# Optimization experiments

Hardware: AMD Instinct MI355X
Metric: run time of the kernel (lower is better)

The kernel has to match this reference:

```python
import jax, jax.numpy as jnp
import numpy as np

VOCAB = 100000; D = 300; F_NUM = 768
M = 64; N = 16
SURF_L = 4; CTX_L = 50; DOC_L = 100; BODY_L = 200
HEADS = 5


def _conv_relu_avg(x, W, b):
    # x: [B, L, D] tokens-embedded; conv1d (valid) + relu + global avgpool -> [B, F]
    y = jax.lax.conv_general_dilated(x.transpose(0, 2, 1), W, (1,), 'VALID',
                                     dimension_numbers=('NCH', 'OIH', 'NCH'))
    return jax.nn.relu(y + b[None, :, None]).mean(axis=2)


def _mha(q, k, v, num_heads=HEADS):
    # split-head scaled dot-product attention (no learned projections), q:[Lq,D] k,v:[Lk,D]
    Lq, Dm = q.shape
    hd = Dm // num_heads
    qh = q.reshape(Lq, num_heads, hd).transpose(1, 0, 2)
    kh = k.reshape(k.shape[0], num_heads, hd).transpose(1, 0, 2)
    vh = v.reshape(v.shape[0], num_heads, hd).transpose(1, 0, 2)
    att = jax.nn.softmax(jnp.einsum('hqd,hkd->hqk', qh, kh) * (1.0 / np.sqrt(hd)), axis=-1)
    out = jnp.einsum('hqk,hkd->hqd', att, vh)
    return out.transpose(1, 0, 2).reshape(Lq, Dm)


def _cos(a, b, eps=1e-6):
    na = jnp.maximum(jnp.sqrt((a * a).sum(-1)), eps)
    nb = jnp.maximum(jnp.sqrt((b * b).sum(-1)), eps)
    return (a * b).sum(-1) / (na * nb)


def setup_inputs() -> dict:
    key = jax.random.key(0)
    ks = jax.random.split(key, 20)
    inp = {}
    inp['mention_entity'] = jnp.ones((M, N), dtype=jnp.int32)
    inp['m'] = M
    inp['n'] = N
    inp['mention_vec'] = jax.random.randint(ks[0], (M, SURF_L), 0, VOCAB)
    inp['context_vec'] = jax.random.randint(ks[1], (M, CTX_L), 0, VOCAB)
    inp['doc_vec'] = jax.random.randint(ks[2], (DOC_L,), 0, VOCAB)
    inp['title_vec'] = jax.random.normal(ks[3], (N, F_NUM), dtype=jnp.float32)
    inp['body_vec'] = jax.random.randint(ks[4], (N, BODY_L), 0, VOCAB)
    inp['sfeats'] = jnp.zeros((N, 1), dtype=jnp.float32)
    inp['m2c_prior'] = jax.random.uniform(ks[5], (N,), dtype=jnp.float32)
    inp['men2cands'] = jax.random.randint(ks[6], (M, N), 0, VOCAB)
    inp['contexts_ids'] = jax.random.randint(ks[7], (M, CTX_L), 0, VOCAB)
    inp['hand_features'] = jax.random.uniform(ks[8], (N, 1), dtype=jnp.float32)
    inp['bert_doc_vec'] = jax.random.normal(ks[9], (1, F_NUM), dtype=jnp.float32)
    # learned parameters
    inp['embed_table'] = jax.random.normal(ks[10], (VOCAB, D), dtype=jnp.float32) * 0.1
    inp['conv_ms_w'] = jax.random.normal(ks[11], (F_NUM, D, 2), dtype=jnp.float32) * 0.05
    inp['conv_ms_b'] = jnp.zeros((F_NUM,), dtype=jnp.float32)
    inp['conv_mc_w'] = jax.random.normal(ks[12], (F_NUM, D, 5), dtype=jnp.float32) * 0.05
    inp['conv_mc_b'] = jnp.zeros((F_NUM,), dtype=jnp.float32)
    inp['layer_local_w'] = jax.random.normal(ks[13], (7,), dtype=jnp.float32) * 0.3
    inp['layer_local_b'] = jnp.zeros((), dtype=jnp.float32)
    inp['att_w1'] = jax.random.normal(ks[14], (600, 300), dtype=jnp.float32) * 0.05
    inp['att_b1'] = jnp.zeros((300,), dtype=jnp.float32)
    inp['att_w2'] = jax.random.normal(ks[15], (300, 1), dtype=jnp.float32) * 0.05
    inp['att_b2'] = jnp.zeros((), dtype=jnp.float32)
    return inp


def reference(mention_entity, m, n, mention_vec, context_vec, doc_vec, title_vec,
              body_vec, sfeats, m2c_prior, men2cands, contexts_ids, hand_features,
              bert_doc_vec, embed_table, conv_ms_w, conv_ms_b, conv_mc_w, conv_mc_b,
              layer_local_w, layer_local_b, att_w1, att_b1, att_w2, att_b2):
    # per-mention conv features (vectorized over all mentions at once)
    ms = _conv_relu_avg(embed_table[mention_vec], conv_ms_w, conv_ms_b)   # [M,768]
    mc = _conv_relu_avg(embed_table[context_vec], conv_mc_w, conv_mc_b)   # [M,768]
    md = bert_doc_vec[0]                                                  # [768]
    doc_emb = embed_table[doc_vec]                                        # [100,300]
    body_emb = embed_table[body_vec]                                      # [N,200,300]

    # per-candidate cross attention doc<->body, max-pooled over query positions
    att_d_b = jax.vmap(lambda b: _mha(doc_emb, b, b).max(axis=0))(body_emb)          # [N,300]
    att_b_d = jax.vmap(lambda b: _mha(b, doc_emb, doc_emb).max(axis=0))(body_emb)    # [N,300]
    comb = jnp.concatenate([att_d_b, att_b_d], axis=-1)                              # [N,600]
    att_score = jax.nn.sigmoid(jax.nn.relu(comb @ att_w1 + att_b1) @ att_w2 + att_b2)[:, 0]  # [N]

    # LocalCtxAttRanker: candidate-vs-context attention score
    ctx_emb = embed_table[contexts_ids]                                   # [M,50,300]
    cand_emb = embed_table[men2cands]                                     # [M,N,300]
    tok = jnp.einsum('mnd,mtd->mnt', cand_emb, ctx_emb)                   # [M,N,50]
    p = jax.nn.softmax(tok.max(axis=1), axis=-1)                          # [M,50]
    ctxv = jnp.einsum('mt,mtd->md', p, ctx_emb)                           # [M,300]
    local_att = jnp.einsum('mnd,md->mn', cand_emb, ctxv)                  # [M,N]

    cos_st = _cos(ms[:, None, :], title_vec[None, :, :])                  # [M,N]
    cos_dt = _cos(md[None, :], title_vec)                                 # [N]
    cos_ct = _cos(mc[:, None, :], title_vec[None, :, :])                  # [M,N]

    Mm = ms.shape[0]
    bc = lambda v: jnp.broadcast_to(v[None, :], (Mm, v.shape[0]))
    # feature order matches torch.cat((hand_fea, prior, localAtt, attScore, C_score))
    feats = jnp.stack([bc(hand_features[:, 0]), bc(m2c_prior), local_att,
                       bc(att_score), cos_st, bc(cos_dt), cos_ct], axis=-1)  # [M,N,7]
    score = feats @ layer_local_w + layer_local_b                         # [M,N]

    # per-mention standardization (unbiased std, as torch.std), softmax and uniform renorm
    mu = score.mean(axis=1, keepdims=True)
    sd = score.std(axis=1, keepdims=True, ddof=1)
    z = (score - mu) / sd
    sm = jax.nn.softmax(z, axis=1)
    zmin = z.min(axis=1, keepdims=True)
    zmax = z.max(axis=1, keepdims=True)
    u = (z + 1.0 - zmin) / (zmax - zmin)
    u = u / u.sum(axis=1, keepdims=True)
    return (z, sm, u)
```

## Files before the change

### kernel.cpp

```cpp
#include <hip/hip_runtime.h>

#define MM 64
#define NN 16
#define DDIM 300
#define FNUM 768
#define SURF_LL 4
#define CTX_LL 50
#define DOC_LL 100
#define BODY_LL 200
#define NHEADS 5
#define HDIM 60

#define GM 2944
#define GK 1536
#define GN 768

typedef unsigned short u16;
typedef unsigned int u32;
typedef __attribute__((ext_vector_type(8))) short short8;
typedef __attribute__((ext_vector_type(4))) float f32x4;

#define OFF_MSG    0
#define OFF_CTX2G  76800
#define OFF_CANDG  1036800
#define OFF_MS     1344000
#define OFF_MC     1393152
#define OFF_PV0    1442304
#define OFF_PV1    1461504
#define OFF_ASC    1495104
#define OFF_LATT   1495120
#define OFF_ABF    1496144
#define OFF_WTMC   (OFF_ABF + GM*GK/2)
#define OFF_WTMS   (OFF_WTMC + GN*GK/2)

__device__ __forceinline__ u16 f2bf(float x) {
  union { float f; u32 u; } v; v.f = x;
  u32 r = v.u + 0x7FFFu + ((v.u >> 16) & 1u);
  return (u16)(r >> 16);
}

__device__ __forceinline__ float rdlane(float x, int l) {
  return __uint_as_float(__builtin_amdgcn_readlane(__float_as_uint(x), l));
}

__global__ __launch_bounds__(256) void mega_prep_kernel(
    const float* __restrict__ embed,
    const int* __restrict__ mention_vec,
    const int* __restrict__ context_vec,
    const int* __restrict__ contexts_ids,
    const int* __restrict__ men2cands,
    const float* __restrict__ Wmc,
    const float* __restrict__ Wms,
    float* __restrict__ dst, float* __restrict__ mc,
    float* __restrict__ att_logit,
    u32* __restrict__ Abf, u32* __restrict__ WTmc, float* __restrict__ WTms) {
  int bid = blockIdx.x;
  if (bid < 5250) {
    int e = bid * 256 + threadIdx.x;
    int row = e / DDIM;
    int col = e - row * DDIM;
    int tok;
    if (row < 256)       tok = mention_vec[row];
    else if (row < 3456) tok = contexts_ids[row - 256];
    else                 tok = men2cands[row - 3456];
    dst[e] = embed[(size_t)tok * DDIM + col];
  } else if (bid < 5442) {
    mc[(bid - 5250) * 256 + threadIdx.x] = 0.f;
  } else if (bid == 5442) {
    if (threadIdx.x < NN) att_logit[threadIdx.x] = 0.f;
  } else if (bid < 14275) {
    int idx = (bid - 5443) * 256 + threadIdx.x;
    int r = idx / (GK / 2);
    int kp = idx - r * (GK / 2);
    int k = kp * 2;
    int m = r / 46, t = r - m * 46;
    u32 out = 0;
#pragma unroll
    for (int j = 0; j < 2; j++) {
      int kj = k + j;
      u16 h = 0;
      if (kj < 1500) {
        int tap = kj / 300;
        int d = kj - tap * 300;
        int tok = context_vec[m * CTX_LL + t + tap];
        h = f2bf(embed[(size_t)tok * DDIM + d]);
      }
      out |= (u32)h << (16 * j);
    }
    Abf[idx] = out;
  } else if (bid < 16579) {
    int idx = (bid - 14275) * 256 + threadIdx.x;
    int n = idx / (GK / 2);
    int kp = idx - n * (GK / 2);
    int k = kp * 2;
    u32 out = 0;
#pragma unroll
    for (int j = 0; j < 2; j++) {
      int kj = k + j;
      u16 h = 0;
      if (kj < 1500) {
        int tap = kj / 300;
        int d = kj - tap * 300;
        h = f2bf(Wmc[(size_t)n * 1500 + d * 5 + tap]);
      }
      out |= (u32)h << (16 * j);
    }
    WTmc[idx] = out;
  } else {
    int idx = (bid - 16579) * 256 + threadIdx.x;
    int k = idx / FNUM;
    int f = idx - k * FNUM;
    WTms[idx] = Wms[(size_t)f * 600 + k];
  }
}

__global__ __launch_bounds__(256) void conv_gemm_kernel(
    const u16* __restrict__ A,
    const u16* __restrict__ B,
    const float* __restrict__ bias,
    float* __restrict__ mc) {
  int bn = blockIdx.x, bm = blockIdx.y;
  __shared__ u16 As[64][72];
  __shared__ u16 Bs[64][72];
  int tid = threadIdx.x;
  int w = tid >> 6, lane = tid & 63;
  int wr = w >> 1, wc = w & 1;
  int lg = lane >> 4, lm = lane & 15;
  f32x4 acc[2][2];
#pragma unroll
  for (int i = 0; i < 2; i++)
#pragma unroll
    for (int j = 0; j < 2; j++) acc[i][j] = (f32x4)0.f;
  int c0row = tid >> 3, ck = (tid & 7) * 8;
  const u16* Ag = A + (size_t)(bm * 64) * GK;
  const u16* Bg = B + (size_t)(bn * 64) * GK;
  for (int kt = 0; kt < GK / 64; kt++) {
    int k0 = kt * 64;
    uint4 av0 = *(const uint4*)(Ag + (size_t)c0row * GK + k0 + ck);
    uint4 av1 = *(const uint4*)(Ag + (size_t)(c0row + 32) * GK + k0 + ck);
    uint4 bv0 = *(const uint4*)(Bg + (size_t)c0row * GK + k0 + ck);
    uint4 bv1 = *(const uint4*)(Bg + (size_t)(c0row + 32) * GK + k0 + ck);
    __syncthreads();
    *(uint4*)&As[c0row][ck] = av0;
    *(uint4*)&As[c0row + 32][ck] = av1;
    *(uint4*)&Bs[c0row][ck] = bv0;
    *(uint4*)&Bs[c0row + 32][ck] = bv1;
    __syncthreads();
#pragma unroll
    for (int kk = 0; kk < 2; kk++) {
      short8 af0 = *(const short8*)&As[wr * 32 + lm][kk * 32 + lg * 8];
      short8 af1 = *(const short8*)&As[wr * 32 + 16 + lm][kk * 32 + lg * 8];
      short8 bf0 = *(const short8*)&Bs[wc * 32 + lm][kk * 32 + lg * 8];
      short8 bf1 = *(const short8*)&Bs[wc * 32 + 16 + lm][kk * 32 + lg * 8];
      acc[0][0] = __builtin_amdgcn_mfma_f32_16x16x32_bf16(af0, bf0, acc[0][0], 0, 0, 0);
      acc[0][1] = __builtin_amdgcn_mfma_f32_16x16x32_bf16(af0, bf1, acc[0][1], 0, 0, 0);
      acc[1][0] = __builtin_amdgcn_mfma_f32_16x16x32_bf16(af1, bf0, acc[1][0], 0, 0, 0);
      acc[1][1] = __builtin_amdgcn_mfma_f32_16x16x32_bf16(af1, bf1, acc[1][1], 0, 0, 0);
    }
  }
#pragma unroll
  for (int mf = 0; mf < 2; mf++)
#pragma unroll
    for (int nf = 0; nf < 2; nf++) {
      int col = bn * 64 + wc * 32 + nf * 16 + lm;
      float bb = bias[col];
      int base = bm * 64 + wr * 32 + mf * 16 + lg * 4;
      int mcur = base / 46;
      float s = 0.f;
#pragma unroll
      for (int r = 0; r < 4; r++) {
        float v = fmaxf(acc[mf][nf][r] + bb, 0.f) * (1.0f / 46.0f);
        int mm = (base + r) / 46;
        if (mm != mcur) { atomicAdd(&mc[mcur * FNUM + col], s); s = 0.f; mcur = mm; }
        s += v;
      }
      atomicAdd(&mc[mcur * FNUM + col], s);
    }
}

__device__ __forceinline__ void conv_ms_body(
    const float* __restrict__ msg, const float* __restrict__ WT,
    const float* __restrict__ B, float* __restrict__ ms, int b) {
  int m = b / 3, fi = b - m * 3;
  int f = fi * 256 + threadIdx.x;
  const float* x = msg + m * SURF_LL * DDIM;
  float a0 = 0.f, a1 = 0.f, a2 = 0.f;
  for (int d = 0; d < DDIM; d++) {
    float v0 = x[d], v1 = x[DDIM + d], v2 = x[2 * DDIM + d], v3 = x[3 * DDIM + d];
    float wA = WT[(size_t)(2 * d) * FNUM + f];
    float wB = WT[(size_t)(2 * d + 1) * FNUM + f];
    a0 += v0 * wA + v1 * wB;
    a1 += v1 * wA + v2 * wB;
    a2 += v2 * wA + v3 * wB;
  }
  float bb = B[f];
  float r = fmaxf(a0 + bb, 0.f) + fmaxf(a1 + bb, 0.f) + fmaxf(a2 + bb, 0.f);
  ms[m * FNUM + f] = r * (1.0f / 3.0f);
}

template <int DIR>
__device__ __forceinline__ void scores_pv_body(
    const float* __restrict__ embed, const int* __restrict__ doc_vec,
    const int* __restrict__ body_vec, float* __restrict__ pvp, int b,
    float* __restrict__ smem) {
  constexpr int Lq = DIR ? 200 : 100;
  constexpr int NT = DIR ? 1 : 2;
  constexpr int NQT = DIR ? 7 : 4;
  int qt = b / 80;
  int rem = b - qt * 80;
  int n = rem / 5, h = rem - n * 5;
  const int* qids = DIR ? body_vec + n * BODY_LL : doc_vec;
  const int* kids = DIR ? doc_vec : body_vec + n * BODY_LL;
  float* Ks = smem;
  float* Qs = smem + 6200;
  float* red = smem + 8248;
  for (int idx = threadIdx.x; idx < 32 * 15; idx += 256) {
    int r = idx / 15, c = idx - r * 15;
    int q = qt * 32 + r; if (q >= Lq) q = Lq - 1;
    float4 v = *(const float4*)(embed + (size_t)qids[q] * DDIM + h * HDIM + c * 4);
    float* dp = Qs + r * 64 + c * 4;
    dp[0] = v.x; dp[1] = v.y; dp[2] = v.z; dp[3] = v.w;
  }
  int w = threadIdx.x >> 6, lane = threadIdx.x & 63;
  int dl = (lane < HDIM) ? lane : (HDIM - 1);
  const float scale = 0.12909944487358056f;
  float mrun[8], srun[8], O[8];
#pragma unroll
  for (int i = 0; i < 8; i++) { mrun[i] = -1e30f; srun[i] = 0.f; O[i] = 0.f; }
  int kc0 = lane;
  int kc1 = (lane + 64 < 100) ? lane + 64 : 99;
  bool v1ok = (lane + 64 < 100);
  for (int kt = 0; kt < NT; kt++) {
    if (kt > 0) __syncthreads();
    for (int idx = threadIdx.x; idx < 100 * 15; idx += 256) {
      int r = idx / 15, c = idx - r * 15;
      float4 v = *(const float4*)(embed + (size_t)kids[kt * 100 + r] * DDIM + h * HDIM + c * 4);
      float* dp = Ks + r * 62 + c * 4;
      dp[0] = v.x; dp[1] = v.y; dp[2] = v.z; dp[3] = v.w;
    }
    __syncthreads();
    float acc[8][2];
#pragma unroll
    for (int i = 0; i < 8; i++) { acc[i][0] = 0.f; acc[i][1] = 0.f; }
    for (int d = 0; d < HDIM; d += 4) {
      float2 a0 = *(const float2*)&Ks[kc0 * 62 + d];
      float2 b0 = *(const float2*)&Ks[kc0 * 62 + d + 2];
      float2 a1 = *(const float2*)&Ks[kc1 * 62 + d];
      float2 b1 = *(const float2*)&Ks[kc1 * 62 + d + 2];
#pragma unroll
      for (int i = 0; i < 8; i++) {
        float4 qv = *(const float4*)&Qs[(w * 8 + i) * 64 + d];
        acc[i][0] += qv.x * a0.x + qv.y * a0.y + qv.z * b0.x + qv.w * b0.y;
        acc[i][1] += qv.x * a1.x + qv.y * a1.y + qv.z * b1.x + qv.w * b1.y;
      }
    }
#pragma unroll
    for (int i = 0; i < 8; i++) {
      float v0 = acc[i][0] * scale;
      float v1 = v1ok ? acc[i][1] * scale : -1e30f;
      float tm = fmaxf(v0, v1);
#pragma unroll
      for (int o = 32; o >= 1; o >>= 1) tm = fmaxf(tm, __shfl_xor(tm, o));
      float mn = fmaxf(mrun[i], tm);
      float fsc = __expf(mrun[i] - mn);
      float p0 = __expf(v0 - mn);
      float p1 = v1ok ? __expf(v1 - mn) : 0.f;
      float ts = p0 + p1;
#pragma unroll
      for (int o = 32; o >= 1; o >>= 1) ts += __shfl_xor(ts, o);
      srun[i] = srun[i] * fsc + ts;
      mrun[i] = mn;
      O[i] *= fsc;
      acc[i][0] = p0; acc[i][1] = p1;
    }
#pragma unroll 4
    for (int k = 0; k < 64; k++) {
      float vk = Ks[k * 62 + dl];
#pragma unroll
      for (int i = 0; i < 8; i++) O[i] += rdlane(acc[i][0], k) * vk;
    }
#pragma unroll 4
    for (int k = 64; k < 100; k++) {
      float vk = Ks[k * 62 + dl];
#pragma unroll
      for (int i = 0; i < 8; i++) O[i] += rdlane(acc[i][1], k - 64) * vk;
    }
  }
  float omax = -1e30f;
#pragma unroll
  for (int i = 0; i < 8; i++) {
    int q = qt * 32 + w * 8 + i;
    if (q < Lq) omax = fmaxf(omax, O[i] / srun[i]);
  }
  red[w * 64 + lane] = omax;
  __syncthreads();
  if (threadIdx.x < 64 && lane < HDIM) {
    float m4 = fmaxf(fmaxf(red[0 * 64 + lane], red[1 * 64 + lane]),
                     fmaxf(red[2 * 64 + lane], red[3 * 64 + lane]));
    pvp[((size_t)(n * NHEADS + h) * NQT + qt) * HDIM + lane] = m4;
  }
}

__device__ __forceinline__ void tokctxv_body(
    const float* __restrict__ candg, const float* __restrict__ ctx2g,
    float* __restrict__ local_att, int m, float* __restrict__ smem) {
  float* ctx   = smem;
  float* tokb  = smem + 4800;
  float* tkmx  = smem + 5072;
  float* pp    = smem + 5136;
  float* sctxv = smem + 5200;
  int tid = threadIdx.x;
  int nI = tid >> 4, tt = tid & 15;
  const float* cand = candg + (size_t)m * NN * DDIM;
  for (int tile = 0; tile < 4; tile++) {
    int cbase = tile * 16;
    __syncthreads();
    for (int i = tid; i < 16 * DDIM; i += 256) {
      int rr = i / DDIM, cc = i - rr * DDIM;
      int t = cbase + rr;
      ctx[rr * DDIM + cc] = (t < CTX_LL) ? ctx2g[(size_t)(m * CTX_LL + t) * DDIM + cc] : 0.f;
    }
    __syncthreads();
    const float4* ca = (const float4*)(cand + nI * DDIM);
    const float4* cb = (const float4*)(ctx + tt * DDIM);
    float dsum = 0.f;
#pragma unroll
    for (int c = 0; c < 75; c++) {
      float4 a = ca[c], b = cb[c];
      dsum += a.x * b.x + a.y * b.y + a.z * b.z + a.w * b.w;
    }
    tokb[nI * 17 + tt] = dsum;
    __syncthreads();
    if (tid < 16) {
      float mx = -1e30f;
      for (int nn = 0; nn < NN; nn++) mx = fmaxf(mx, tokb[nn * 17 + tid]);
      int t = cbase + tid;
      if (t < CTX_LL) tkmx[t] = mx;
    }
  }
  __syncthreads();
  if (tid < 64) {
    float v = (tid < CTX_LL) ? tkmx[tid] : -1e30f;
    float mx = v;
#pragma unroll
    for (int o = 32; o >= 1; o >>= 1) mx = fmaxf(mx, __shfl_xor(mx, o));
    float e = (tid < CTX_LL) ? expf(v - mx) : 0.f;
    float s = e;
#pragma unroll
    for (int o = 32; o >= 1; o >>= 1) s += __shfl_xor(s, o);
    pp[tid] = e / s;
  }
  __syncthreads();
  for (int d = tid; d < DDIM; d += 256) {
    float acc = 0.f;
    for (int t = 0; t < CTX_LL; t++)
      acc += pp[t] * ctx2g[(size_t)(m * CTX_LL + t) * DDIM + d];
    sctxv[d] = acc;
  }
  __syncthreads();
  int j = tid & 15;
  float dd = 0.f;
  for (int i = j; i < DDIM; i += 16) dd += cand[nI * DDIM + i] * sctxv[i];
#pragma unroll
  for (int o = 8; o >= 1; o >>= 1) dd += __shfl_xor(dd, o);
  if (j == 0) local_att[m * NN + nI] = dd;
}

__global__ __launch_bounds__(256, 4) void mega_mid_kernel(
    const float* __restrict__ embed,
    const int* __restrict__ doc_vec,
    const int* __restrict__ body_vec,
    const float* __restrict__ msg,
    const float* __restrict__ WTms,
    const float* __restrict__ Bms,
    const float* __restrict__ candg,
    const float* __restrict__ ctx2g,
    float* __restrict__ ms,
    float* __restrict__ pv0,
    float* __restrict__ pv1,
    float* __restrict__ local_att) {
  __shared__ float smem[8504];
  int bid = blockIdx.x;
  if (bid < 192) {
    conv_ms_body(msg, WTms, Bms, ms, bid);
  } else if (bid < 512) {
    scores_pv_body<0>(embed, doc_vec, body_vec, pv0, bid - 192, smem);
  } else if (bid < 1072) {
    scores_pv_body<1>(embed, doc_vec, body_vec, pv1, bid - 512, smem);
  } else {
    tokctxv_body(candg, ctx2g, local_att, bid - 1072, smem);
  }
}

__global__ __launch_bounds__(256) void mlp_kernel(
    const float* __restrict__ pv0, const float* __restrict__ pv1,
    const float* __restrict__ w1, const float* __restrict__ b1,
    const float* __restrict__ w2,
    float* __restrict__ att_logit) {
  int bid = blockIdx.x;
  int n = bid / 5, jc = bid - n * 5;
  int tid = threadIdx.x;
  __shared__ float comb[600];
  __shared__ float partial[4][64];
  for (int idx = tid; idx < 600; idx += 256) {
    int side = idx >= 300;
    int pos = idx - side * 300;
    int h = pos / 60, d = pos - h * 60;
    float mx = -1e30f;
    if (!side) {
#pragma unroll
      for (int pt = 0; pt < 4; pt++)
        mx = fmaxf(mx, pv0[(size_t)((n * NHEADS + h) * 4 + pt) * HDIM + d]);
    } else {
#pragma unroll
      for (int pt = 0; pt < 7; pt++)
        mx = fmaxf(mx, pv1[(size_t)((n * NHEADS + h) * 7 + pt) * HDIM + d]);
    }
    comb[idx] = mx;
  }
  __syncthreads();
  int w = tid >> 6, lane = tid & 63;
  int jl = (lane < 60) ? lane : 59;
  int jg = jc * 60 + jl;
  float acc = 0.f;
  for (int k = w; k < 600; k += 4)
    acc += comb[k] * w1[(size_t)k * 300 + jg];
  partial[w][lane] = acc;
  __syncthreads();
  if (tid < 64) {
    float hv = partial[0][lane] + partial[1][lane] +
               partial[2][lane] + partial[3][lane];
    float hj = fmaxf(hv + b1[jg], 0.f) * w2[jg];
    if (lane >= 60) hj = 0.f;
#pragma unroll
    for (int o = 32; o >= 1; o >>= 1) hj += __shfl_xor(hj, o);
    if (lane == 0) atomicAdd(&att_logit[n], hj);
  }
}

__global__ __launch_bounds__(256) void final_kernel(
    const float* __restrict__ ms,
    const float* __restrict__ mc,
    const float* __restrict__ title,
    const float* __restrict__ bert,
    const float* __restrict__ att_logit,
    const float* __restrict__ b2,
    const float* __restrict__ m2c_prior,
    const float* __restrict__ hand,
    const float* __restrict__ local_att,
    const float* __restrict__ w7,
    const float* __restrict__ b7,
    float* __restrict__ out) {
  int m = blockIdx.x, tid = threadIdx.x;
  __shared__ float sms[FNUM], smc[FNUM], smd[FNUM];
  __shared__ float snorm[3], sscore[16], wred[3][4];
  for (int i = tid; i < FNUM; i += 256) {
    sms[i] = ms[m * FNUM + i];
    smc[i] = mc[m * FNUM + i];
    smd[i] = bert[i];
  }
  __syncthreads();
  float p1 = 0.f, p2 = 0.f, p3 = 0.f;
  for (int i = tid; i < FNUM; i += 256) {
    float a = sms[i], b = smc[i], c = smd[i];
    p1 += a * a; p2 += b * b; p3 += c * c;
  }
#pragma unroll
  for (int o = 32; o >= 1; o >>= 1) {
    p1 += __shfl_xor(p1, o); p2 += __shfl_xor(p2, o); p3 += __shfl_xor(p3, o);
  }
  int wid = tid >> 6, lane = tid & 63;
  if (lane == 0) { wred[0][wid] = p1; wred[1][wid] = p2; wred[2][wid] = p3; }
  __syncthreads();
  if (tid == 0) {
    snorm[0] = fmaxf(sqrtf(wred[0][0] + wred[0][1] + wred[0][2] + wred[0][3]), 1e-6f);
    snorm[1] = fmaxf(sqrtf(wred[1][0] + wred[1][1] + wred[1][2] + wred[1][3]), 1e-6f);
    snorm[2] = fmaxf(sqrtf(wred[2][0] + wred[2][1] + wred[2][2] + wred[2][3]), 1e-6f);
  }
  __syncthreads();
  int nI = tid >> 4, j = tid & 15;
  float d1 = 0.f, d2 = 0.f, d3 = 0.f, d4 = 0.f;
  for (int i = j; i < FNUM; i += 16) {
    float t = title[nI * FNUM + i];
    d1 += sms[i] * t; d2 += smc[i] * t; d3 += smd[i] * t; d4 += t * t;
  }
#pragma unroll
  for (int o = 8; o >= 1; o >>= 1) {
    d1 += __shfl_xor(d1, o); d2 += __shfl_xor(d2, o);
    d3 += __shfl_xor(d3, o); d4 += __shfl_xor(d4, o);
  }
  if (j == 0) {
    float nt = fmaxf(sqrtf(d4), 1e-6f);
    float cos_st = d1 / (snorm[0] * nt);
    float cos_ct = d2 / (snorm[1] * nt);
    float cos_dt = d3 / (snorm[2] * nt);
    float asc = 1.0f / (1.0f + expf(-(att_logit[nI] + b2[0])));
    float score = hand[nI] * w7[0] + m2c_prior[nI] * w7[1] +
                  local_att[m * NN + nI] * w7[2] + asc * w7[3] +
                  cos_st * w7[4] + cos_dt * w7[5] + cos_ct * w7[6] + b7[0];
    sscore[nI] = score;
  }
  __syncthreads();
  if (tid < 16) {
    float x = sscore[tid];
    float s = x;
#pragma unroll
    for (int o = 8; o >= 1; o >>= 1) s += __shfl_xor(s, o);
    float mu = s * (1.0f / 16.0f);
    float dv = (x - mu) * (x - mu);
    float vs = dv;
#pragma unroll
    for (int o = 8; o >= 1; o >>= 1) vs += __shfl_xor(vs, o);
    float sd = sqrtf(vs * (1.0f / 15.0f));
    float z = (x - mu) / sd;
    float zm = z;
#pragma unroll
    for (int o = 8; o >= 1; o >>= 1) zm = fmaxf(zm, __shfl_xor(zm, o));
    float e = expf(z - zm);
    float es = e;
#pragma unroll
    for (int o = 8; o >= 1; o >>= 1) es += __shfl_xor(es, o);
    float sm = e / es;
    float zmin = z;
#pragma unroll
    for (int o = 8; o >= 1; o >>= 1) zmin = fminf(zmin, __shfl_xor(zmin, o));
    float u0 = (z + 1.0f - zmin) / (zm - zmin);
    float us = u0;
#pragma unroll
    for (int o = 8; o >= 1; o >>= 1) us += __shfl_xor(us, o);
    float u = u0 / us;
    out[m * NN + tid] = z;
    out[MM * NN + m * NN + tid] = sm;
    out[2 * MM * NN + m * NN + tid] = u;
  }
}

extern "C" void kernel_launch(void* const* d_in, const int* in_sizes, int n_in,
                              void* d_out, int out_size, void* d_ws, size_t ws_size,
                              hipStream_t stream) {
  const int*   mention_vec   = (const int*)d_in[3];
  const int*   context_vec   = (const int*)d_in[4];
  const int*   doc_vec       = (const int*)d_in[5];
  const float* title_vec     = (const float*)d_in[6];
  const int*   body_vec      = (const int*)d_in[7];
  const float* m2c_prior     = (const float*)d_in[9];
  const int*   men2cands     = (const int*)d_in[10];
  const int*   contexts_ids  = (const int*)d_in[11];
  const float* hand_features = (const float*)d_in[12];
  const float* bert_doc_vec  = (const float*)d_in[13];
  const float* embed_table   = (const float*)d_in[14];
  const float* conv_ms_w     = (const float*)d_in[15];
  const float* conv_ms_b     = (const float*)d_in[16];
  const float* conv_mc_w     = (const float*)d_in[17];
  const float* conv_mc_b     = (const float*)d_in[18];
  const float* layer_local_w = (const float*)d_in[19];
  const float* layer_local_b = (const float*)d_in[20];
  const float* att_w1        = (const float*)d_in[21];
  const float* att_b1        = (const float*)d_in[22];
  const float* att_w2        = (const float*)d_in[23];
  const float* att_b2        = (const float*)d_in[24];

  float* ws     = (float*)d_ws;
  float* msg    = ws + OFF_MSG;
  float* ctx2g  = ws + OFF_CTX2G;
  float* candg  = ws + OFF_CANDG;
  float* ms     = ws + OFF_MS;
  float* mc     = ws + OFF_MC;
  float* pv0    = ws + OFF_PV0;
  float* pv1    = ws + OFF_PV1;
  float* att_lg = ws + OFF_ASC;
  float* latt   = ws + OFF_LATT;
  u16*   Abf    = (u16*)(ws + OFF_ABF);
  u16*   WTmc   = (u16*)(ws + OFF_WTMC);
  float* WTms   = ws + OFF_WTMS;
  float* out    = (float*)d_out;

  mega_prep_kernel<<<dim3(18379), dim3(256), 0, stream>>>(
      embed_table, mention_vec, context_vec, contexts_ids, men2cands,
      conv_mc_w, conv_ms_w, ws, mc, att_lg, (u32*)Abf, (u32*)WTmc, WTms);
  conv_gemm_kernel<<<dim3(GN / 64, GM / 64), dim3(256), 0, stream>>>(
      Abf, WTmc, conv_mc_b, mc);
  mega_mid_kernel<<<dim3(1136), dim3(256), 0, stream>>>(
      embed_table, doc_vec, body_vec, msg, WTms, conv_ms_b, candg, ctx2g,
      ms, pv0, pv1, latt);
  mlp_kernel<<<dim3(80), dim3(256), 0, stream>>>(
      pv0, pv1, att_w1, att_b1, att_w2, att_lg);
  final_kernel<<<dim3(MM), dim3(256), 0, stream>>>(
      ms, mc, title_vec, bert_doc_vec, att_lg, att_b2, m2c_prior,
      hand_features, latt, layer_local_w, layer_local_b, out);
}
```

Baseline: 439.3 us.

## Replace online softmax and readlane PV with two-pass softmax and LDS-staged probabilities

The attention body now computes all QK scores before any softmax, holding every score tile in registers. It then does a single exact softmax normalization and runs the PV product by staging the probabilities in shared memory (reusing the Q buffer) and reading them back as float4, instead of broadcasting each one with readlane. The aim is to drop the per-tile rescaling and the serial readlane chains. In exchange it reloads the first K tile for the second pass, adds extra barriers, and removes the occupancy hint from launch_bounds, which may raise register pressure.

```diff
diff --git a/kernel.cpp b/kernel.cpp
--- a/kernel.cpp
+++ b/kernel.cpp
@@ -37,10 +37,6 @@
   union { float f; u32 u; } v; v.f = x;
   u32 r = v.u + 0x7FFFu + ((v.u >> 16) & 1u);
   return (u16)(r >> 16);
-}
-
-__device__ __forceinline__ float rdlane(float x, int l) {
-  return __uint_as_float(__builtin_amdgcn_readlane(__float_as_uint(x), l));
 }
 
 __global__ __launch_bounds__(256) void mega_prep_kernel(
@@ -198,6 +194,42 @@
   ms[m * FNUM + f] = r * (1.0f / 3.0f);
 }
 
+#define PV_TILE(S0, S1)                                                       \
+  {                                                                           \
+    if (lane < 52) {                                                          \
+      _Pragma("unroll") for (int i = 0; i < 8; i++)                           \
+          Pl[(w * 8 + i) * 52 + lane] = acc[i][S0];                           \
+    }                                                                         \
+    _Pragma("unroll 4") for (int k4 = 0; k4 < 13; k4++) {                     \
+      float kv0 = Ks[(k4 * 4 + 0) * 62 + dl];                                 \
+      float kv1 = Ks[(k4 * 4 + 1) * 62 + dl];                                 \
+      float kv2 = Ks[(k4 * 4 + 2) * 62 + dl];                                 \
+      float kv3 = Ks[(k4 * 4 + 3) * 62 + dl];                                 \
+      _Pragma("unroll") for (int i = 0; i < 8; i++) {                         \
+        float4 pq = *(const float4*)&Pl[(w * 8 + i) * 52 + k4 * 4];           \
+        O[i] += pq.x * kv0 + pq.y * kv1 + pq.z * kv2 + pq.w * kv3;            \
+      }                                                                       \
+    }                                                                         \
+    if (lane >= 52) {                                                         \
+      _Pragma("unroll") for (int i = 0; i < 8; i++)                           \
+          Pl[(w * 8 + i) * 52 + (lane - 52)] = acc[i][S0];                    \
+    }                                                                         \
+    if (k1ok) {                                                               \
+      _Pragma("unroll") for (int i = 0; i < 8; i++)                           \
+          Pl[(w * 8 + i) * 52 + (lane + 12)] = acc[i][S1];                    \
+    }                                                                         \
+    _Pragma("unroll 4") for (int k4 = 0; k4 < 12; k4++) {                     \
+      float kv0 = Ks[(52 + k4 * 4 + 0) * 62 + dl];                            \
+      float kv1 = Ks[(52 + k4 * 4 + 1) * 62 + dl];                            \
+      float kv2 = Ks[(52 + k4 * 4 + 2) * 62 + dl];                            \
+      float kv3 = Ks[(52 + k4 * 4 + 3) * 62 + dl];                            \
+      _Pragma("unroll") for (int i = 0; i < 8; i++) {                         \
+        float4 pq = *(const float4*)&Pl[(w * 8 + i) * 52 + k4 * 4];           \
+        O[i] += pq.x * kv0 + pq.y * kv1 + pq.z * kv2 + pq.w * kv3;            \
+      }                                                                       \
+    }                                                                         \
+  }
+
 template <int DIR>
 __device__ __forceinline__ void scores_pv_body(
     const float* __restrict__ embed, const int* __restrict__ doc_vec,
@@ -205,6 +237,7 @@
     float* __restrict__ smem) {
   constexpr int Lq = DIR ? 200 : 100;
   constexpr int NT = DIR ? 1 : 2;
+  constexpr int NS = 2 * NT;
   constexpr int NQT = DIR ? 7 : 4;
   int qt = b / 80;
   int rem = b - qt * 80;
@@ -213,6 +246,7 @@
   const int* kids = DIR ? doc_vec : body_vec + n * BODY_LL;
   float* Ks = smem;
   float* Qs = smem + 6200;
+  float* Pl = smem + 6200;
   float* red = smem + 8248;
   for (int idx = threadIdx.x; idx < 32 * 15; idx += 256) {
     int r = idx / 15, c = idx - r * 15;
@@ -221,27 +255,44 @@
     float* dp = Qs + r * 64 + c * 4;
     dp[0] = v.x; dp[1] = v.y; dp[2] = v.z; dp[3] = v.w;
   }
+  for (int idx = threadIdx.x; idx < 100 * 15; idx += 256) {
+    int r = idx / 15, c = idx - r * 15;
+    float4 v = *(const float4*)(embed + (size_t)kids[r] * DDIM + h * HDIM + c * 4);
+    float* dp = Ks + r * 62 + c * 4;
+    dp[0] = v.x; dp[1] = v.y; dp[2] = v.z; dp[3] = v.w;
+  }
+  __syncthreads();
   int w = threadIdx.x >> 6, lane = threadIdx.x & 63;
   int dl = (lane < HDIM) ? lane : (HDIM - 1);
-  const float scale = 0.12909944487358056f;
-  float mrun[8], srun[8], O[8];
-#pragma unroll
-  for (int i = 0; i < 8; i++) { mrun[i] = -1e30f; srun[i] = 0.f; O[i] = 0.f; }
   int kc0 = lane;
-  int kc1 = (lane + 64 < 100) ? lane + 64 : 99;
-  bool v1ok = (lane + 64 < 100);
-  for (int kt = 0; kt < NT; kt++) {
-    if (kt > 0) __syncthreads();
+  bool k1ok = (lane < 36);
+  int kc1 = k1ok ? lane + 64 : 99;
+  float acc[8][NS];
+#pragma unroll
+  for (int i = 0; i < 8; i++)
+#pragma unroll
+    for (int j = 0; j < NS; j++) acc[i][j] = 0.f;
+  for (int d = 0; d < HDIM; d += 4) {
+    float2 a0 = *(const float2*)&Ks[kc0 * 62 + d];
+    float2 b0 = *(const float2*)&Ks[kc0 * 62 + d + 2];
+    float2 a1 = *(const float2*)&Ks[kc1 * 62 + d];
+    float2 b1 = *(const float2*)&Ks[kc1 * 62 + d + 2];
+#pragma unroll
+    for (int i = 0; i < 8; i++) {
+      float4 qv = *(const float4*)&Qs[(w * 8 + i) * 64 + d];
+      acc[i][0] += qv.x * a0.x + qv.y * a0.y + qv.z * b0.x + qv.w * b0.y;
+      acc[i][1] += qv.x * a1.x + qv.y * a1.y + qv.z * b1.x + qv.w * b1.y;
+    }
+  }
+  if constexpr (NT == 2) {
+    __syncthreads();
     for (int idx = threadIdx.x; idx < 100 * 15; idx += 256) {
       int r = idx / 15, c = idx - r * 15;
-      float4 v = *(const float4*)(embed + (size_t)kids[kt * 100 + r] * DDIM + h * HDIM + c * 4);
+      float4 v = *(const float4*)(embed + (size_t)kids[100 + r] * DDIM + h * HDIM + c * 4);
       float* dp = Ks + r * 62 + c * 4;
       dp[0] = v.x; dp[1] = v.y; dp[2] = v.z; dp[3] = v.w;
     }
     __syncthreads();
-    float acc[8][2];
-#pragma unroll
-    for (int i = 0; i < 8; i++) { acc[i][0] = 0.f; acc[i][1] = 0.f; }
     for (int d = 0; d < HDIM; d += 4) {
       float2 a0 = *(const float2*)&Ks[kc0 * 62 + d];
       float2 b0 = *(const float2*)&Ks[kc0 * 62 + d + 2];
@@ -250,47 +301,60 @@
 #pragma unroll
       for (int i = 0; i < 8; i++) {
         float4 qv = *(const float4*)&Qs[(w * 8 + i) * 64 + d];
-        acc[i][0] += qv.x * a0.x + qv.y * a0.y + qv.z * b0.x + qv.w * b0.y;
-        acc[i][1] += qv.x * a1.x + qv.y * a1.y + qv.z * b1.x + qv.w * b1.y;
+        acc[i][NS - 2] += qv.x * a0.x + qv.y * a0.y + qv.z * b0.x + qv.w * b0.y;
+        acc[i][NS - 1] += qv.x * a1.x + qv.y * a1.y + qv.z * b1.x + qv.w * b1.y;
       }
     }
-#pragma unroll
-    for (int i = 0; i < 8; i++) {
-      float v0 = acc[i][0] * scale;
-      float v1 = v1ok ? acc[i][1] * scale : -1e30f;
-      float tm = fmaxf(v0, v1);
-#pragma unroll
-      for (int o = 32; o >= 1; o >>= 1) tm = fmaxf(tm, __shfl_xor(tm, o));
-      float mn = fmaxf(mrun[i], tm);
-      float fsc = __expf(mrun[i] - mn);
-      float p0 = __expf(v0 - mn);
-      float p1 = v1ok ? __expf(v1 - mn) : 0.f;
-      float ts = p0 + p1;
-#pragma unroll
-      for (int o = 32; o >= 1; o >>= 1) ts += __shfl_xor(ts, o);
-      srun[i] = srun[i] * fsc + ts;
-      mrun[i] = mn;
-      O[i] *= fsc;
-      acc[i][0] = p0; acc[i][1] = p1;
-    }
-#pragma unroll 4
-    for (int k = 0; k < 64; k++) {
-      float vk = Ks[k * 62 + dl];
-#pragma unroll
-      for (int i = 0; i < 8; i++) O[i] += rdlane(acc[i][0], k) * vk;
-    }
-#pragma unroll 4
-    for (int k = 64; k < 100; k++) {
-      float vk = Ks[k * 62 + dl];
-#pragma unroll
-      for (int i = 0; i < 8; i++) O[i] += rdlane(acc[i][1], k - 64) * vk;
-    }
+  }
+  const float scale = 0.12909944487358056f;
+#pragma unroll
+  for (int i = 0; i < 8; i++) {
+    float mx = acc[i][0];
+    if (k1ok) mx = fmaxf(mx, acc[i][1]);
+    if constexpr (NT == 2) {
+      mx = fmaxf(mx, acc[i][2]);
+      if (k1ok) mx = fmaxf(mx, acc[i][3]);
+    }
+#pragma unroll
+    for (int o = 32; o >= 1; o >>= 1) mx = fmaxf(mx, __shfl_xor(mx, o));
+    float mxs = mx * scale;
+    float p0 = __expf(acc[i][0] * scale - mxs);
+    float p1 = k1ok ? __expf(acc[i][1] * scale - mxs) : 0.f;
+    float s = p0 + p1;
+    float p2 = 0.f, p3 = 0.f;
+    if constexpr (NT == 2) {
+      p2 = __expf(acc[i][2] * scale - mxs);
+      p3 = k1ok ? __expf(acc[i][3] * scale - mxs) : 0.f;
+      s += p2 + p3;
+    }
+#pragma unroll
+    for (int o = 32; o >= 1; o >>= 1) s += __shfl_xor(s, o);
+    float inv = 1.0f / s;
+    acc[i][0] = p0 * inv;
+    acc[i][1] = p1 * inv;
+    if constexpr (NT == 2) { acc[i][2] = p2 * inv; acc[i][3] = p3 * inv; }
+  }
+  __syncthreads();
+  float O[8];
+#pragma unroll
+  for (int i = 0; i < 8; i++) O[i] = 0.f;
+  PV_TILE(NS - 2, NS - 1);
+  if constexpr (NT == 2) {
+    __syncthreads();
+    for (int idx = threadIdx.x; idx < 100 * 15; idx += 256) {
+      int r = idx / 15, c = idx - r * 15;
+      float4 v = *(const float4*)(embed + (size_t)kids[r] * DDIM + h * HDIM + c * 4);
+      float* dp = Ks + r * 62 + c * 4;
+      dp[0] = v.x; dp[1] = v.y; dp[2] = v.z; dp[3] = v.w;
+    }
+    __syncthreads();
+    PV_TILE(0, 1);
   }
   float omax = -1e30f;
 #pragma unroll
   for (int i = 0; i < 8; i++) {
     int q = qt * 32 + w * 8 + i;
-    if (q < Lq) omax = fmaxf(omax, O[i] / srun[i]);
+    if (q < Lq) omax = fmaxf(omax, O[i]);
   }
   red[w * 64 + lane] = omax;
   __syncthreads();
@@ -366,7 +430,7 @@
   if (j == 0) local_att[m * NN + nI] = dd;
 }
 
-__global__ __launch_bounds__(256, 4) void mega_mid_kernel(
+__global__ __launch_bounds__(256) void mega_mid_kernel(
     const float* __restrict__ embed,
     const int* __restrict__ doc_vec,
     const int* __restrict__ body_vec,
```

New measurement: 452.7 us. 3.1% more time.
